# Performance work log

Measured on AMD Instinct MI355X. Metric: run time of the kernel, lower is better.

The kernel has to match this reference:

```python
import jax, jax.numpy as jnp
import numpy as np


def setup_inputs() -> dict:
    key = jax.random.key(0)
    k1, k2, k3, k4, k5 = jax.random.split(key, 5)
    B, D, T = 32, 256, 32       # batch, word_feature_dim, seq_len
    Dh, H, Wd = 128, 128, 128   # image_feature_dim, height, width
    word_features = jax.random.normal(k1, (B, D, T), dtype=jnp.float32)
    image_features = jax.random.normal(k2, (B, Dh, H, Wd), dtype=jnp.float32)
    words_mask = jax.random.randint(k3, (B, T), 0, 2, dtype=jnp.int32)
    W = jax.random.normal(k4, (Dh, D), dtype=jnp.float32) * (1.0 / np.sqrt(D))
    b = jax.random.normal(k5, (Dh,), dtype=jnp.float32) * 0.01
    return {"word_features": word_features, "image_features": image_features,
            "words_mask": words_mask, "W": W, "b": b}


def reference(word_features, image_features, words_mask, W, b):
    B, D, T = word_features.shape
    Dh = image_features.shape[1]
    N = image_features.shape[2] * image_features.shape[3]  # H*W
    # values = fc(word_features^T)^T : [B, Dh, T]
    values = jnp.einsum('bdt,kd->bkt', word_features, W) + b[None, :, None]
    # queries: [B, N, Dh] (flatten spatial)
    queries = image_features.reshape(B, Dh, N)
    # scores S: [B, N, T]
    S = jnp.einsum('bkn,bkt->bnt', queries, values)
    mask = (words_mask != 0)[:, None, :]  # [B,1,T], True => masked
    S = jnp.where(mask, -jnp.inf, S)
    # softmax over seq dim (original: exp / sum(exp)); stable form is same math
    attn_coefficients = jax.nn.softmax(S, axis=2)  # [B, N, T]
    # context vectors: [B, Dh, N]
    attn = jnp.einsum('bkt,bnt->bkn', values, attn_coefficients)
    return attn, attn_coefficients
```

## Files before the change

### kernel.cpp

```cpp
#include <hip/hip_runtime.h>
#include <math.h>

constexpr int Bc  = 32;
constexpr int Dc  = 256;
constexpr int Tc  = 32;
constexpr int DHc = 128;
constexpr int Nc  = 16384;

__global__ __launch_bounds__(256) void values_kernel(
    const float* __restrict__ wf, const float* __restrict__ Wm,
    const float* __restrict__ bias, float* __restrict__ values)
{
    int id = blockIdx.x * 256 + threadIdx.x;
    int t = id & (Tc - 1);
    int k = (id >> 5) & (DHc - 1);
    int b = id >> 12;
    const float* wrow = Wm + (size_t)k * Dc;
    const float* wfp  = wf + (size_t)b * Dc * Tc + t;
    float acc = bias[k];
    #pragma unroll 8
    for (int d = 0; d < Dc; ++d)
        acc = fmaf(wrow[d], wfp[(size_t)d * Tc], acc);
    values[id] = acc;
}

__global__ __launch_bounds__(256) void attn_kernel(
    const float* __restrict__ img, const float* __restrict__ values,
    const int* __restrict__ mask, float* __restrict__ attn,
    float* __restrict__ coeff)
{
    __shared__ float Vs[DHc * Tc];
    __shared__ float mneg[Tc];

    const int tid  = threadIdx.x;
    const int b    = blockIdx.x >> 5;
    const int tile = blockIdx.x & 31;

    {
        const float4* vg = (const float4*)(values + (size_t)b * DHc * Tc);
        float4* vs = (float4*)Vs;
        #pragma unroll
        for (int i = 0; i < 4; ++i) vs[i * 256 + tid] = vg[i * 256 + tid];
    }
    if (tid < Tc) mneg[tid] = mask[b * Tc + tid] ? -INFINITY : 0.0f;
    __syncthreads();

    const int n = tile * 512 + tid * 2;
    const float* qp = img + (size_t)b * DHc * Nc + n;

    float s0[Tc], s1[Tc];
    #pragma unroll
    for (int t = 0; t < Tc; ++t) { s0[t] = 0.0f; s1[t] = 0.0f; }

    #pragma unroll 2
    for (int k = 0; k < DHc; ++k) {
        const float2 q = *(const float2*)(qp + (size_t)k * Nc);
        const float4* vrow = (const float4*)(Vs + k * Tc);
        #pragma unroll
        for (int tt = 0; tt < 8; ++tt) {
            const float4 v = vrow[tt];
            s0[4*tt+0] = fmaf(q.x, v.x, s0[4*tt+0]);
            s0[4*tt+1] = fmaf(q.x, v.y, s0[4*tt+1]);
            s0[4*tt+2] = fmaf(q.x, v.z, s0[4*tt+2]);
            s0[4*tt+3] = fmaf(q.x, v.w, s0[4*tt+3]);
            s1[4*tt+0] = fmaf(q.y, v.x, s1[4*tt+0]);
            s1[4*tt+1] = fmaf(q.y, v.y, s1[4*tt+1]);
            s1[4*tt+2] = fmaf(q.y, v.z, s1[4*tt+2]);
            s1[4*tt+3] = fmaf(q.y, v.w, s1[4*tt+3]);
        }
    }

    float m0 = -INFINITY, m1 = -INFINITY;
    #pragma unroll
    for (int t = 0; t < Tc; ++t) {
        s0[t] += mneg[t]; s1[t] += mneg[t];
        m0 = fmaxf(m0, s0[t]); m1 = fmaxf(m1, s1[t]);
    }
    float sum0 = 0.0f, sum1 = 0.0f;
    #pragma unroll
    for (int t = 0; t < Tc; ++t) {
        s0[t] = __expf(s0[t] - m0); sum0 += s0[t];
        s1[t] = __expf(s1[t] - m1); sum1 += s1[t];
    }
    const float inv0 = 1.0f / sum0, inv1 = 1.0f / sum1;
    #pragma unroll
    for (int t = 0; t < Tc; ++t) { s0[t] *= inv0; s1[t] *= inv1; }

    {
        float4* cp = (float4*)(coeff + ((size_t)b * Nc + n) * Tc);
        #pragma unroll
        for (int tt = 0; tt < 8; ++tt)
            cp[tt] = make_float4(s0[4*tt+0], s0[4*tt+1], s0[4*tt+2], s0[4*tt+3]);
        #pragma unroll
        for (int tt = 0; tt < 8; ++tt)
            cp[8+tt] = make_float4(s1[4*tt+0], s1[4*tt+1], s1[4*tt+2], s1[4*tt+3]);
    }

    float* ap = attn + (size_t)b * DHc * Nc + n;
    #pragma unroll 2
    for (int k = 0; k < DHc; ++k) {
        const float4* vrow = (const float4*)(Vs + k * Tc);
        float a0 = 0.f, b0 = 0.f, c0 = 0.f, d0 = 0.f;
        float a1 = 0.f, b1 = 0.f, c1 = 0.f, d1 = 0.f;
        #pragma unroll
        for (int tt = 0; tt < 8; ++tt) {
            const float4 v = vrow[tt];
            a0 = fmaf(v.x, s0[4*tt+0], a0);
            b0 = fmaf(v.y, s0[4*tt+1], b0);
            c0 = fmaf(v.z, s0[4*tt+2], c0);
            d0 = fmaf(v.w, s0[4*tt+3], d0);
            a1 = fmaf(v.x, s1[4*tt+0], a1);
            b1 = fmaf(v.y, s1[4*tt+1], b1);
            c1 = fmaf(v.z, s1[4*tt+2], c1);
            d1 = fmaf(v.w, s1[4*tt+3], d1);
        }
        *(float2*)(ap + (size_t)k * Nc) =
            make_float2((a0 + b0) + (c0 + d0), (a1 + b1) + (c1 + d1));
    }
}

extern "C" void kernel_launch(void* const* d_in, const int* in_sizes, int n_in,
                              void* d_out, int out_size, void* d_ws, size_t ws_size,
                              hipStream_t stream)
{
    const float* wf   = (const float*)d_in[0];
    const float* img  = (const float*)d_in[1];
    const int*   msk  = (const int*)d_in[2];
    const float* Wm   = (const float*)d_in[3];
    const float* bias = (const float*)d_in[4];

    float* attn  = (float*)d_out;
    float* coeff = attn + (size_t)Bc * DHc * Nc;
    float* vals  = (float*)d_ws;

    values_kernel<<<(Bc * DHc * Tc) / 256, 256, 0, stream>>>(wf, Wm, bias, vals);
    attn_kernel<<<(Bc * Nc) / 512, 256, 0, stream>>>(img, vals, msk, attn, coeff);
}
```

Baseline: 613.3 us.

## Use split-fp16 MFMA for score and context matmuls in attention kernel

Replaces the per-thread FP32 FMA loops with 16x16x32 fp16 MFMA instructions, splitting values and queries into high and low fp16 parts to approximate FP32 accuracy. Softmax is done on MFMA output fragments with cross-lane shuffles, and probabilities are reshuffled into an MFMA operand layout for the context product. The aim is to remove the vector-ALU compute bottleneck and register pressure. It risks precision loss because probabilities are rounded to fp16 without a low part, and it changes the global access patterns.

```diff
diff --git a/kernel.cpp b/kernel.cpp
--- a/kernel.cpp
+++ b/kernel.cpp
@@ -6,6 +6,10 @@
 constexpr int Tc  = 32;
 constexpr int DHc = 128;
 constexpr int Nc  = 16384;
+
+typedef _Float16 v8hf __attribute__((ext_vector_type(8)));
+typedef _Float16 v2hf __attribute__((ext_vector_type(2)));
+typedef float    v4f  __attribute__((ext_vector_type(4)));
 
 __global__ __launch_bounds__(256) void values_kernel(
     const float* __restrict__ wf, const float* __restrict__ Wm,
@@ -24,98 +28,155 @@
     values[id] = acc;
 }
 
+__device__ __forceinline__ _Float16 pick_half(int u, int sel) {
+    unsigned short s = (unsigned short)(sel ? (u >> 16) : u);
+    return __builtin_bit_cast(_Float16, s);
+}
+
 __global__ __launch_bounds__(256) void attn_kernel(
     const float* __restrict__ img, const float* __restrict__ values,
     const int* __restrict__ mask, float* __restrict__ attn,
     float* __restrict__ coeff)
 {
-    __shared__ float Vs[DHc * Tc];
+    constexpr int VT_LD = 136;
+    constexpr int VP_LD = 40;
+    __shared__ _Float16 VTh[Tc * VT_LD];
+    __shared__ _Float16 VTl[Tc * VT_LD];
+    __shared__ _Float16 VPh[DHc * VP_LD];
+    __shared__ _Float16 VPl[DHc * VP_LD];
     __shared__ float mneg[Tc];
 
-    const int tid  = threadIdx.x;
-    const int b    = blockIdx.x >> 5;
-    const int tile = blockIdx.x & 31;
+    const int tid   = threadIdx.x;
+    const int b     = blockIdx.x >> 5;
+    const int strip = blockIdx.x & 31;
 
     {
-        const float4* vg = (const float4*)(values + (size_t)b * DHc * Tc);
-        float4* vs = (float4*)Vs;
+        const float* vb = values + (size_t)b * DHc * Tc;
         #pragma unroll
-        for (int i = 0; i < 4; ++i) vs[i * 256 + tid] = vg[i * 256 + tid];
+        for (int i = 0; i < 16; ++i) {
+            int idx = tid + 256 * i;
+            int k = idx >> 5, t = idx & 31;
+            float v = vb[idx];
+            _Float16 vh = (_Float16)v;
+            _Float16 vl = (_Float16)(v - (float)vh);
+            VTh[t * VT_LD + k] = vh;
+            VTl[t * VT_LD + k] = vl;
+            VPh[k * VP_LD + t] = vh;
+            VPl[k * VP_LD + t] = vl;
+        }
+        if (tid < Tc) mneg[tid] = mask[b * Tc + tid] ? -INFINITY : 0.0f;
     }
-    if (tid < Tc) mneg[tid] = mask[b * Tc + tid] ? -INFINITY : 0.0f;
     __syncthreads();
 
-    const int n = tile * 512 + tid * 2;
-    const float* qp = img + (size_t)b * DHc * Nc + n;
+    const int lane = tid & 63;
+    const int wave = tid >> 6;
+    const int c    = lane & 15;
+    const int g    = lane >> 4;
 
-    float s0[Tc], s1[Tc];
+    float madd[2][4];
     #pragma unroll
-    for (int t = 0; t < Tc; ++t) { s0[t] = 0.0f; s1[t] = 0.0f; }
+    for (int tt = 0; tt < 2; ++tt)
+        #pragma unroll
+        for (int r = 0; r < 4; ++r)
+            madd[tt][r] = mneg[16 * tt + 4 * g + r];
 
-    #pragma unroll 2
-    for (int k = 0; k < DHc; ++k) {
-        const float2 q = *(const float2*)(qp + (size_t)k * Nc);
-        const float4* vrow = (const float4*)(Vs + k * Tc);
+    const float* qbase = img  + ((size_t)b * DHc + 8 * g) * Nc + c;
+    float*       abase = attn + ((size_t)b * DHc + 4 * g) * Nc + c;
+    float*       cbase = coeff + (size_t)b * Nc * Tc;
+
+    const int ls_lo = c + 32 * (g & 1);
+    const int sel   = g >> 1;
+
+    for (int it = 0; it < 8; ++it) {
+        const int n0 = strip * 512 + (it * 4 + wave) * 16;
+
+        float q[4][8];
+        const float* qp = qbase + n0;
         #pragma unroll
-        for (int tt = 0; tt < 8; ++tt) {
-            const float4 v = vrow[tt];
-            s0[4*tt+0] = fmaf(q.x, v.x, s0[4*tt+0]);
-            s0[4*tt+1] = fmaf(q.x, v.y, s0[4*tt+1]);
-            s0[4*tt+2] = fmaf(q.x, v.z, s0[4*tt+2]);
-            s0[4*tt+3] = fmaf(q.x, v.w, s0[4*tt+3]);
-            s1[4*tt+0] = fmaf(q.y, v.x, s1[4*tt+0]);
-            s1[4*tt+1] = fmaf(q.y, v.y, s1[4*tt+1]);
-            s1[4*tt+2] = fmaf(q.y, v.z, s1[4*tt+2]);
-            s1[4*tt+3] = fmaf(q.y, v.w, s1[4*tt+3]);
+        for (int ks = 0; ks < 4; ++ks)
+            #pragma unroll
+            for (int j = 0; j < 8; ++j)
+                q[ks][j] = qp[(size_t)(ks * 32 + j) * Nc];
+
+        v8hf Qh[4], Ql[4];
+        #pragma unroll
+        for (int ks = 0; ks < 4; ++ks)
+            #pragma unroll
+            for (int j = 0; j < 8; ++j) {
+                _Float16 h = (_Float16)q[ks][j];
+                Qh[ks][j] = h;
+                Ql[ks][j] = (_Float16)(q[ks][j] - (float)h);
+            }
+
+        v4f Sh[2], Sl[2];
+        #pragma unroll
+        for (int tt = 0; tt < 2; ++tt) {
+            Sh[tt] = (v4f){0.f, 0.f, 0.f, 0.f};
+            Sl[tt] = (v4f){0.f, 0.f, 0.f, 0.f};
         }
-    }
+        #pragma unroll
+        for (int tt = 0; tt < 2; ++tt) {
+            const int rowbase = (16 * tt + c) * VT_LD + 8 * g;
+            #pragma unroll
+            for (int ks = 0; ks < 4; ++ks) {
+                v8hf va = *(const v8hf*)&VTh[rowbase + ks * 32];
+                v8hf vl = *(const v8hf*)&VTl[rowbase + ks * 32];
+                Sh[tt] = __builtin_amdgcn_mfma_f32_16x16x32_f16(va, Qh[ks], Sh[tt], 0, 0, 0);
+                Sl[tt] = __builtin_amdgcn_mfma_f32_16x16x32_f16(va, Ql[ks], Sl[tt], 0, 0, 0);
+                Sl[tt] = __builtin_amdgcn_mfma_f32_16x16x32_f16(vl, Qh[ks], Sl[tt], 0, 0, 0);
+            }
+        }
 
-    float m0 = -INFINITY, m1 = -INFINITY;
-    #pragma unroll
-    for (int t = 0; t < Tc; ++t) {
-        s0[t] += mneg[t]; s1[t] += mneg[t];
-        m0 = fmaxf(m0, s0[t]); m1 = fmaxf(m1, s1[t]);
-    }
-    float sum0 = 0.0f, sum1 = 0.0f;
-    #pragma unroll
-    for (int t = 0; t < Tc; ++t) {
-        s0[t] = __expf(s0[t] - m0); sum0 += s0[t];
-        s1[t] = __expf(s1[t] - m1); sum1 += s1[t];
-    }
-    const float inv0 = 1.0f / sum0, inv1 = 1.0f / sum1;
-    #pragma unroll
-    for (int t = 0; t < Tc; ++t) { s0[t] *= inv0; s1[t] *= inv1; }
+        float p0[4], p1[4];
+        float m = -INFINITY;
+        #pragma unroll
+        for (int r = 0; r < 4; ++r) {
+            p0[r] = Sh[0][r] + Sl[0][r] + madd[0][r];
+            p1[r] = Sh[1][r] + Sl[1][r] + madd[1][r];
+            m = fmaxf(m, fmaxf(p0[r], p1[r]));
+        }
+        m = fmaxf(m, __shfl_xor(m, 16));
+        m = fmaxf(m, __shfl_xor(m, 32));
+        float sum = 0.0f;
+        #pragma unroll
+        for (int r = 0; r < 4; ++r) {
+            p0[r] = __expf(p0[r] - m); sum += p0[r];
+            p1[r] = __expf(p1[r] - m); sum += p1[r];
+        }
+        sum += __shfl_xor(sum, 16);
+        sum += __shfl_xor(sum, 32);
+        const float inv = 1.0f / sum;
+        #pragma unroll
+        for (int r = 0; r < 4; ++r) { p0[r] *= inv; p1[r] *= inv; }
 
-    {
-        float4* cp = (float4*)(coeff + ((size_t)b * Nc + n) * Tc);
+        float* cp = cbase + (size_t)(n0 + c) * Tc + 4 * g;
+        *(float4*)cp        = make_float4(p0[0], p0[1], p0[2], p0[3]);
+        *(float4*)(cp + 16) = make_float4(p1[0], p1[1], p1[2], p1[3]);
+
+        v8hf Pb;
         #pragma unroll
-        for (int tt = 0; tt < 8; ++tt)
-            cp[tt] = make_float4(s0[4*tt+0], s0[4*tt+1], s0[4*tt+2], s0[4*tt+3]);
+        for (int r = 0; r < 4; ++r) {
+            v2hf h2; h2[0] = (_Float16)p0[r]; h2[1] = (_Float16)p1[r];
+            int u   = __builtin_bit_cast(int, h2);
+            int ulo = __shfl(u, ls_lo);
+            int uhi = __shfl(u, ls_lo + 16);
+            Pb[r]     = pick_half(ulo, sel);
+            Pb[4 + r] = pick_half(uhi, sel);
+        }
+
         #pragma unroll
-        for (int tt = 0; tt < 8; ++tt)
-            cp[8+tt] = make_float4(s1[4*tt+0], s1[4*tt+1], s1[4*tt+2], s1[4*tt+3]);
-    }
-
-    float* ap = attn + (size_t)b * DHc * Nc + n;
-    #pragma unroll 2
-    for (int k = 0; k < DHc; ++k) {
-        const float4* vrow = (const float4*)(Vs + k * Tc);
-        float a0 = 0.f, b0 = 0.f, c0 = 0.f, d0 = 0.f;
-        float a1 = 0.f, b1 = 0.f, c1 = 0.f, d1 = 0.f;
-        #pragma unroll
-        for (int tt = 0; tt < 8; ++tt) {
-            const float4 v = vrow[tt];
-            a0 = fmaf(v.x, s0[4*tt+0], a0);
-            b0 = fmaf(v.y, s0[4*tt+1], b0);
-            c0 = fmaf(v.z, s0[4*tt+2], c0);
-            d0 = fmaf(v.w, s0[4*tt+3], d0);
-            a1 = fmaf(v.x, s1[4*tt+0], a1);
-            b1 = fmaf(v.y, s1[4*tt+1], b1);
-            c1 = fmaf(v.z, s1[4*tt+2], c1);
-            d1 = fmaf(v.w, s1[4*tt+3], d1);
+        for (int mt = 0; mt < 8; ++mt) {
+            const int vrow = (16 * mt + c) * VP_LD + 8 * g;
+            v8hf va  = *(const v8hf*)&VPh[vrow];
+            v8hf vb2 = *(const v8hf*)&VPl[vrow];
+            v4f o = (v4f){0.f, 0.f, 0.f, 0.f};
+            o = __builtin_amdgcn_mfma_f32_16x16x32_f16(va,  Pb, o, 0, 0, 0);
+            o = __builtin_amdgcn_mfma_f32_16x16x32_f16(vb2, Pb, o, 0, 0, 0);
+            float* ap = abase + (size_t)(16 * mt) * Nc + n0;
+            #pragma unroll
+            for (int r = 0; r < 4; ++r)
+                ap[(size_t)r * Nc] = o[r];
         }
-        *(float2*)(ap + (size_t)k * Nc) =
-            make_float2((a0 + b0) + (c0 + d0), (a1 + b1) + (c1 + d1));
     }
 }
 
@@ -134,5 +195,5 @@
     float* vals  = (float*)d_ws;
 
     values_kernel<<<(Bc * DHc * Tc) / 256, 256, 0, stream>>>(wf, Wm, bias, vals);
-    attn_kernel<<<(Bc * Nc) / 512, 256, 0, stream>>>(img, vals, msk, attn, coeff);
+    attn_kernel<<<Bc * 32, 256, 0, stream>>>(img, vals, msk, attn, coeff);
 }
```

After: 563.0 us. 8.2% less time.
